# Kernel optimization log

Measured on AMD Instinct MI355X. Metric: run time of the kernel, lower is better.

Reference implementation:

```python
import jax, jax.numpy as jnp
import numpy as np

B, T, N, DM, H, DK, DH = 2, 12, 207, 64, 4, 16, 256


def _build_D_pos(num_heads, length):
    # RetNet-style decay matrix D[h,n,m] = r_h^(n-m) for n>=m, column-sqrt-sum normalized
    r = 1.0 - 2.0 ** (-5.0 - jnp.arange(num_heads, dtype=jnp.float32))
    idx = jnp.arange(length)
    diff = idx[:, None] - idx[None, :]
    mask = diff >= 0
    safe = jnp.where(mask, diff, 0).astype(jnp.float32)
    D = jnp.where(mask, r[:, None, None] ** safe, 0.0)  # [H,T,T]
    D = D / jnp.sqrt(jnp.sum(D, axis=-1, keepdims=True))
    n = jnp.arange(1, length + 1, dtype=jnp.float32)  # theta = 1
    pos = jnp.stack([jnp.cos(n), jnp.sin(n)], axis=0)  # [2,T] = [real, imag]
    return D, pos


def setup_inputs() -> dict:
    key = jax.random.key(0)
    ks = jax.random.split(key, 12)
    xav = lambda k, fi, fo, shp: jax.random.normal(k, shp, jnp.float32) * np.sqrt(2.0 / (fi + fo)).astype(np.float32)
    out2 = 3 * H * DK * DM  # 12288
    return {
        "inputs": jax.random.normal(ks[0], (B, T, N, DM), jnp.float32),
        "c_inputs": jax.random.normal(ks[1], (B, T, N, DM), jnp.float32),
        "ml_w1": xav(ks[2], DM, DH, (DM, DH)),
        "ml_b1": jnp.zeros((DH,), jnp.float32),
        "ml_w2": xav(ks[3], DH, out2, (DH, out2)),
        "ml_b2": jnp.zeros((out2,), jnp.float32),
        "gdc_w1": xav(ks[4], DK, DM, (H, DK, DM)),
        "gdc_w2": xav(ks[5], DK, DM, (H, DK, DM)),
        "wg_w": xav(ks[6], DM, DM, (DM, DM)),
        "wg_b": jnp.zeros((DM,), jnp.float32),
        "wo_w": xav(ks[7], DM, DM, (DM, DM)),
        "wo_b": jnp.zeros((DM,), jnp.float32),
        "ln_g": jnp.ones((DM,), jnp.float32),
        "ln_b": jnp.zeros((DM,), jnp.float32),
        "Num": 0,
    }


def reference(inputs, c_inputs, ml_w1, ml_b1, ml_w2, ml_b2, gdc_w1, gdc_w2,
              wg_w, wg_b, wo_w, wo_b, ln_g, ln_b, Num):
    b, t, n, dm = inputs.shape
    h, dk, _ = gdc_w1.shape
    D, pos = _build_D_pos(h, t)

    # MetaLearner: per-token QKV weight matrices [B,T,N,3,H,dk,dm]
    hid = jax.nn.relu(c_inputs @ ml_w1 + ml_b1)
    W = (hid @ ml_w2 + ml_b2).reshape(b, t, n, 3, h, dk, dm)
    Q = jnp.einsum('btnhkd,btnd->btnhk', W[:, :, :, 0], inputs)
    K = jnp.einsum('btnhkd,btnd->btnhk', W[:, :, :, 1], inputs)
    V = jnp.einsum('btnhkd,btnd->btnhk', W[:, :, :, 2], inputs)

    # complex rotary-like position scaling: leading dim c=2 (real/imag)
    posb = pos[:, :t].reshape(2, 1, t, 1, 1, 1)
    Qp = Q[None] * posb  # [2,B,T,N,H,dk]
    Kp = K[None] * posb

    # retention: sum over c of QK^T / sqrt(dk), decay-masked, abs-sum normalized
    scores = jnp.einsum('cbtnhk,cbsnhk->bnhts', Qp, Kp) / jnp.sqrt(jnp.float32(dk))
    ret = scores * D[None, None]  # [B,N,H,T,T]
    den = jnp.maximum(jnp.abs(jnp.sum(ret, axis=-1, keepdims=True)), 1.0)
    ret = ret / den
    out = jnp.einsum('bnhts,bsnhk->bhtnk', ret, V)  # [B,H,T,N,dk]

    # GroupNorm: normalize over last (dk) axis, nan -> 0
    mu = jnp.mean(out, axis=-1, keepdims=True)
    var = jnp.var(out, axis=-1, keepdims=True)
    out = (out - mu) / jnp.sqrt(var)
    out = jnp.where(jnp.isnan(out), 0.0, out)

    out = 3.0 * jnp.tanh(jnp.swapaxes(out, 0, 1))  # [H,B,T,N,dk]

    # Gated_Dynamic_Connection: softmax over heads per output channel
    x = jnp.transpose(out, (1, 2, 3, 0, 4))  # [B,T,N,H,dk]
    a = jnp.einsum('btnhk,hkm->btnhm', x, gdc_w1)
    s = jax.nn.softmax(jax.nn.relu(jnp.einsum('btnhk,hkm->btnhm', x, gdc_w2)), axis=3)
    g = jnp.einsum('btnhm,btnhm->btnm', a, s)  # [B,T,N,dm]

    # Swish gate + output projection
    z = (inputs @ wg_w + wg_b) * g
    z = z * jax.nn.sigmoid(z)
    o = z @ wo_w + wo_b

    # residual + LayerNorm
    y = o + inputs
    mu2 = jnp.mean(y, axis=-1, keepdims=True)
    var2 = jnp.var(y, axis=-1, keepdims=True)
    y = (y - mu2) / jnp.sqrt(var2 + 1e-5) * ln_g + ln_b
    return y
```

## Files before the change

### kernel.cpp

```cpp
#include <hip/hip_runtime.h>
#include <math.h>

#define B_ 2
#define T_ 12
#define N_ 207
#define DM_ 64
#define H_ 4
#define DK_ 16
#define DH_ 256
#define MTOK 4968
#define MTOKP 4992
#define OUT2 12288
#define QKVC 192
#define RW 512

typedef __bf16 bf16x8 __attribute__((ext_vector_type(8)));
typedef float f32x4 __attribute__((ext_vector_type(4)));
typedef unsigned short ushortx8 __attribute__((ext_vector_type(8)));

__device__ __forceinline__ unsigned short f2bf(float f) {
    union { float f; unsigned u; } v; v.f = f;
    unsigned r = v.u + 0x7fffu + ((v.u >> 16) & 1u);
    return (unsigned short)(r >> 16);
}
__device__ __forceinline__ float bf2f(unsigned short b) {
    union { unsigned u; float f; } v; v.u = ((unsigned)b) << 16; return v.f;
}
__device__ __forceinline__ void gll16(const void* g, void* l) {
    __builtin_amdgcn_global_load_lds((const __attribute__((address_space(1))) void*)g,
                                     (__attribute__((address_space(3))) void*)l, 16, 0, 0);
}

__global__ __launch_bounds__(256) void k_hid2(const float* __restrict__ cin,
                                              const float* __restrict__ w1,
                                              const float* __restrict__ b1,
                                              unsigned short* __restrict__ hid_i) {
    __shared__ float cs[16][DM_];
    const int t0 = blockIdx.x * 16;
    const int tid = threadIdx.x;
    #pragma unroll
    for (int r = 0; r < 4; ++r) {
        int idx = r * 256 + tid;
        int t = idx >> 6, d = idx & 63;
        int tok = t0 + t;
        cs[t][d] = (tok < MTOK) ? cin[(size_t)tok * DM_ + d] : 0.f;
    }
    __syncthreads();
    float a[16];
    #pragma unroll
    for (int t = 0; t < 16; ++t) a[t] = 0.f;
    for (int d = 0; d < DM_; ++d) {
        float wv = w1[d * DH_ + tid];
        #pragma unroll
        for (int t = 0; t < 16; ++t) a[t] = fmaf(cs[t][d], wv, a[t]);
    }
    float b = b1[tid];
    const int g = tid >> 3, pos = tid & 7;
    #pragma unroll
    for (int t = 0; t < 16; ++t) {
        int tok = t0 + t;
        float val = (tok < MTOK) ? fmaxf(a[t] + b, 0.f) : 0.f;
        unsigned short hi = f2bf(val);
        hid_i[(size_t)tok * RW + g * 16 + pos]     = hi;
        hid_i[(size_t)tok * RW + g * 16 + 8 + pos] = f2bf(val - bf2f(hi));
    }
}

__global__ __launch_bounds__(256) void k_split(const float* __restrict__ w2,
                                               unsigned short* __restrict__ wi) {
    __shared__ float tbuf[64][72];
    const int tid = threadIdx.x;
    const int c0 = blockIdx.x * 64;
    const int j0 = blockIdx.y * 64;
    #pragma unroll
    for (int r = 0; r < 4; ++r) {
        int idx = r * 256 + tid;
        int j = idx >> 4, c4 = idx & 15;
        float4 v = *reinterpret_cast<const float4*>(w2 + (size_t)(j0 + j) * OUT2 + c0 + c4 * 4);
        *reinterpret_cast<float4*>(&tbuf[j][c4 * 4]) = v;
    }
    __syncthreads();
    #pragma unroll
    for (int r = 0; r < 2; ++r) {
        int slot = r * 256 + tid;
        int c = slot >> 3, j8 = slot & 7;
        ushortx8 Hv, Lv;
        #pragma unroll
        for (int e = 0; e < 8; ++e) {
            float f = tbuf[j8 * 8 + e][c];
            unsigned short h = f2bf(f);
            Hv[e] = h;
            Lv[e] = f2bf(f - bf2f(h));
        }
        size_t off = (size_t)(c0 + c) * RW + (size_t)(j0 + j8 * 8) * 2;
        *reinterpret_cast<ushortx8*>(wi + off)     = Hv;
        *reinterpret_cast<ushortx8*>(wi + off + 8) = Lv;
    }
}

__global__ __launch_bounds__(256, 4) void k_gemm(const unsigned short* __restrict__ Ai,
                                                 const unsigned short* __restrict__ Bi,
                                                 const float* __restrict__ b2,
                                                 const float* __restrict__ x,
                                                 float* __restrict__ qkv) {
    __shared__ __align__(16) unsigned short sA[8192], sB[8192];
    const int tid = threadIdx.x;
    const int bid = blockIdx.x;
    const int xcd = bid & 7;
    const int r_ = bid >> 3;
    const int m0 = (r_ / 12) * 128;
    const int n0 = (xcd * 12 + (r_ % 12)) * 128;
    const int wid = tid >> 6;
    const int lane = tid & 63;
    const int l15 = lane & 15, l4 = lane >> 4;
    const int wm = wid >> 1, wn = wid & 1;

    const int srow = tid >> 3;
    const int sch  = tid & 7;
    const int gch  = sch ^ (srow & 7);
    const unsigned short* pA = Ai + (size_t)(m0 + srow) * RW + gch * 8;
    const unsigned short* pB = Bi + (size_t)(n0 + srow) * RW + gch * 8;
    const size_t rstep = (size_t)32 * RW;
    const int lbase = wid * 512;

    const int rsw = l15 & 7;
    const int chHi = ((2 * l4) ^ rsw) * 8;
    const int chLo = ((2 * l4 + 1) ^ rsw) * 8;

    f32x4 acc[4][4];
    const f32x4 zero = {0.f, 0.f, 0.f, 0.f};
    #pragma unroll
    for (int i = 0; i < 4; ++i)
        #pragma unroll
        for (int j = 0; j < 4; ++j) acc[i][j] = zero;

    for (int ks = 0; ks < 8; ++ks) {
        #pragma unroll
        for (int i = 0; i < 4; ++i) gll16(pA + i * rstep, &sA[i * 2048 + lbase]);
        #pragma unroll
        for (int i = 0; i < 4; ++i) gll16(pB + i * rstep, &sB[i * 2048 + lbase]);
        pA += 64; pB += 64;
        __syncthreads();

        bf16x8 ah[4], al[4];
        #pragma unroll
        for (int mi = 0; mi < 4; ++mi) {
            int rb = (wm * 64 + mi * 16 + l15) * 64;
            ah[mi] = *reinterpret_cast<const bf16x8*>(&sA[rb + chHi]);
            al[mi] = *reinterpret_cast<const bf16x8*>(&sA[rb + chLo]);
        }
        #pragma unroll
        for (int ni = 0; ni < 4; ++ni) {
            int nb = (wn * 64 + ni * 16 + l15) * 64;
            bf16x8 bh = *reinterpret_cast<const bf16x8*>(&sB[nb + chHi]);
            bf16x8 bl = *reinterpret_cast<const bf16x8*>(&sB[nb + chLo]);
            #pragma unroll
            for (int mi = 0; mi < 4; ++mi)
                acc[mi][ni] = __builtin_amdgcn_mfma_f32_16x16x32_bf16(ah[mi], bh, acc[mi][ni], 0, 0, 0);
            #pragma unroll
            for (int mi = 0; mi < 4; ++mi)
                acc[mi][ni] = __builtin_amdgcn_mfma_f32_16x16x32_bf16(ah[mi], bl, acc[mi][ni], 0, 0, 0);
            #pragma unroll
            for (int mi = 0; mi < 4; ++mi)
                acc[mi][ni] = __builtin_amdgcn_mfma_f32_16x16x32_bf16(al[mi], bh, acc[mi][ni], 0, 0, 0);
        }
        __syncthreads();
    }

    const int cg = (n0 >> 6) + wn;
    float b2v[4];
    #pragma unroll
    for (int ni = 0; ni < 4; ++ni) b2v[ni] = b2[cg * 64 + ni * 16 + l15];
    #pragma unroll
    for (int mi = 0; mi < 4; ++mi) {
        #pragma unroll
        for (int r = 0; r < 4; ++r) {
            int rl = wm * 64 + mi * 16 + l4 * 4 + r;
            int gm = m0 + rl;
            int gmc = gm < MTOK ? gm : MTOK - 1;
            float v = 0.f;
            #pragma unroll
            for (int ni = 0; ni < 4; ++ni)
                v = fmaf(acc[mi][ni][r] + b2v[ni], x[(size_t)gmc * DM_ + ni * 16 + l15], v);
            #pragma unroll
            for (int sw = 1; sw < 16; sw <<= 1) v += __shfl_xor(v, sw, 16);
            if (l15 == 0 && gm < MTOK) qkv[(size_t)gm * QKVC + cg] = v;
        }
    }
}

__global__ __launch_bounds__(256) void k_ret4(const float* __restrict__ qkv,
                                              float* __restrict__ xt) {
    const int tid = threadIdx.x;
    const int g = tid >> 6, lane = tid & 63;
    const int n = blockIdx.x * 4 + g;
    const int h = blockIdx.y;
    const int b = blockIdx.z;
    const bool act = (n < N_);
    __shared__ float Q[4][T_][DK_ + 1], K[4][T_][DK_ + 1], V[4][T_][DK_ + 1];
    __shared__ float ret[4][T_][T_ + 1];
    __shared__ float den[4][T_];
    if (act) {
        for (int idx = lane; idx < T_ * DK_; idx += 64) {
            int t = idx >> 4, k = idx & 15;
            size_t base = ((size_t)((b * T_ + t) * N_ + n)) * QKVC + h * DK_ + k;
            Q[g][t][k] = qkv[base];
            K[g][t][k] = qkv[base + 64];
            V[g][t][k] = qkv[base + 128];
        }
        const float r = 1.f - exp2f(-5.f - (float)h);
        for (int p = lane; p < T_ * T_; p += 64) {
            int t = p / T_, s = p - t * T_;
            float val = 0.f;
            if (s <= t) {
                float dot = 0.f;
                #pragma unroll
                for (int k = 0; k < DK_; ++k) dot = fmaf(Q[g][t][k], K[g][s][k], dot);
                float sum = 0.f, rp = 1.f;
                for (int i = 0; i <= t; ++i) { sum += rp; rp *= r; }
                float Dv = powf(r, (float)(t - s)) / sqrtf(sum);
                val = dot * 0.25f * cosf((float)(t - s)) * Dv;
            }
            ret[g][t][s] = val;
        }
        if (lane < T_) {
            float sm = 0.f;
            for (int j = 0; j < T_; ++j) sm += ret[g][lane][j];
            den[g][lane] = fmaxf(fabsf(sm), 1.f);
        }
        for (int idx = lane; idx < T_ * DK_; idx += 64) {
            int t = idx >> 4, k = idx & 15;
            float o = 0.f;
            for (int s = 0; s <= t; ++s) o = fmaf(ret[g][t][s], V[g][s][k], o);
            o /= den[g][t];
            float mu = o;
            #pragma unroll
            for (int w = 8; w >= 1; w >>= 1) mu += __shfl_xor(mu, w, 16);
            mu *= (1.f / 16.f);
            float dv = o - mu;
            float var = dv * dv;
            #pragma unroll
            for (int w = 8; w >= 1; w >>= 1) var += __shfl_xor(var, w, 16);
            var *= (1.f / 16.f);
            float val = dv / sqrtf(var);
            if (isnan(val)) val = 0.f;
            val = 3.f * tanhf(val);
            xt[((size_t)((b * T_ + t) * N_ + n)) * DM_ + h * DK_ + k] = val;
        }
    }
}

__global__ __launch_bounds__(256) void k_out4(const float* __restrict__ xt,
                                              const float* __restrict__ in,
                                              const float* __restrict__ gw1,
                                              const float* __restrict__ gw2,
                                              const float* __restrict__ wgw,
                                              const float* __restrict__ wgb,
                                              const float* __restrict__ wow,
                                              const float* __restrict__ wob,
                                              const float* __restrict__ lng,
                                              const float* __restrict__ lnb,
                                              float* __restrict__ out) {
    const int tid = threadIdx.x;
    const int w = tid >> 6;
    const int m = tid & 63;
    const int tok = blockIdx.x * 4 + w;
    const bool act = tok < MTOK;
    const int tokc = act ? tok : MTOK - 1;
    __shared__ float xsh[4][DM_], insh[4][DM_], zsh[4][DM_];
    xsh[w][m]  = xt[(size_t)tokc * DM_ + m];
    insh[w][m] = in[(size_t)tokc * DM_ + m];
    float ah[H_], sh[H_];
    #pragma unroll
    for (int h = 0; h < H_; ++h) {
        float a = 0.f, s = 0.f;
        #pragma unroll
        for (int k = 0; k < DK_; ++k) {
            float xv = xsh[w][h * DK_ + k];
            a = fmaf(xv, gw1[(h * DK_ + k) * DM_ + m], a);
            s = fmaf(xv, gw2[(h * DK_ + k) * DM_ + m], s);
        }
        ah[h] = a;
        sh[h] = fmaxf(s, 0.f);
    }
    float mx = fmaxf(fmaxf(sh[0], sh[1]), fmaxf(sh[2], sh[3]));
    float e0 = expf(sh[0] - mx), e1 = expf(sh[1] - mx);
    float e2 = expf(sh[2] - mx), e3 = expf(sh[3] - mx);
    float esum = e0 + e1 + e2 + e3;
    float g = (ah[0] * e0 + ah[1] * e1 + ah[2] * e2 + ah[3] * e3) / esum;
    float z = 0.f;
    for (int d = 0; d < DM_; ++d) z = fmaf(insh[w][d], wgw[d * DM_ + m], z);
    z += wgb[m];
    z *= g;
    z = z / (1.f + expf(-z));
    zsh[w][m] = z;
    float o = 0.f;
    for (int d = 0; d < DM_; ++d) o = fmaf(zsh[w][d], wow[d * DM_ + m], o);
    o += wob[m];
    float y = o + insh[w][m];
    float mu = y;
    #pragma unroll
    for (int xm = 32; xm >= 1; xm >>= 1) mu += __shfl_xor(mu, xm, 64);
    mu *= (1.f / 64.f);
    float dv = y - mu;
    float var = dv * dv;
    #pragma unroll
    for (int xm = 32; xm >= 1; xm >>= 1) var += __shfl_xor(var, xm, 64);
    var *= (1.f / 64.f);
    float res = dv / sqrtf(var + 1e-5f) * lng[m] + lnb[m];
    if (act) out[(size_t)tok * DM_ + m] = res;
}

__global__ __launch_bounds__(256) void k_hid(const float* __restrict__ cin,
                                             const float* __restrict__ w1,
                                             const float* __restrict__ b1,
                                             float* __restrict__ hid) {
    __shared__ float cs[4][DM_];
    const int t0 = blockIdx.x * 4;
    const int tid = threadIdx.x;
    {
        int t = tid >> 6, d = tid & 63;
        cs[t][d] = cin[(size_t)(t0 + t) * DM_ + d];
    }
    __syncthreads();
    float a0 = 0.f, a1 = 0.f, a2 = 0.f, a3 = 0.f;
    for (int d = 0; d < DM_; ++d) {
        float w = w1[d * DH_ + tid];
        a0 = fmaf(cs[0][d], w, a0);
        a1 = fmaf(cs[1][d], w, a1);
        a2 = fmaf(cs[2][d], w, a2);
        a3 = fmaf(cs[3][d], w, a3);
    }
    float b = b1[tid];
    hid[(size_t)(t0 + 0) * DH_ + tid] = fmaxf(a0 + b, 0.f);
    hid[(size_t)(t0 + 1) * DH_ + tid] = fmaxf(a1 + b, 0.f);
    hid[(size_t)(t0 + 2) * DH_ + tid] = fmaxf(a2 + b, 0.f);
    hid[(size_t)(t0 + 3) * DH_ + tid] = fmaxf(a3 + b, 0.f);
}

#define BM 192
#define BN 96
template <int KS>
__global__ __launch_bounds__(256, 2) void k_qkv(const float* __restrict__ x,
                                                const float* __restrict__ hid,
                                                const float* __restrict__ w2,
                                                const float* __restrict__ b2,
                                                float* __restrict__ part) {
    constexpr int JPB = DH_ / KS;
    __shared__ float4 xs4[BM * 16];
    __shared__ float4 ws4[BN * 16];
    const int tid = threadIdx.x;
    const int m0 = blockIdx.x * BM;
    const int c0 = blockIdx.y * BN;
    const int kz = blockIdx.z;
    const int cidx = tid & 15;
    const int midx = tid >> 4;
    #pragma unroll
    for (int i = 0; i < 12; ++i) {
        int e4 = tid + 256 * i;
        int m = e4 >> 4;
        int d4 = e4 & 15;
        int gm = m0 + m;
        float4 v = make_float4(0.f, 0.f, 0.f, 0.f);
        if (gm < MTOK) v = *reinterpret_cast<const float4*>(x + (size_t)gm * DM_ + d4 * 4);
        xs4[m * 16 + (d4 ^ (m & 15))] = v;
    }
    float acc[12][6];
    #pragma unroll
    for (int i = 0; i < 12; ++i)
        #pragma unroll
        for (int q = 0; q < 6; ++q) acc[i][q] = 0.f;
    const int jn = (kz == 0) ? (JPB + 1) : JPB;
    float4 st[6];
    {
        const float* src = w2 + (size_t)(kz * JPB) * OUT2 + c0 * DM_;
        #pragma unroll
        for (int i = 0; i < 6; ++i)
            st[i] = *reinterpret_cast<const float4*>(src + (tid + 256 * i) * 4);
    }
    #pragma unroll
    for (int i = 0; i < 6; ++i) {
        int t4 = tid + 256 * i;
        int c = t4 >> 4;
        int d4 = t4 & 15;
        ws4[c * 16 + (d4 ^ (c & 15))] = st[i];
    }
    __syncthreads();
    for (int jj = 0; jj < jn; ++jj) {
        const bool have_next = (jj + 1 < jn);
        if (have_next) {
            const bool nb = (kz == 0) && (jj + 1 == JPB);
            const float* src = nb ? (b2 + c0 * DM_)
                                  : (w2 + (size_t)(kz * JPB + jj + 1) * OUT2 + c0 * DM_);
            #pragma unroll
            for (int i = 0; i < 6; ++i)
                st[i] = *reinterpret_cast<const float4*>(src + (tid + 256 * i) * 4);
        }
        const bool bias_cur = (kz == 0) && (jj == JPB);
        const int jg = kz * JPB + jj;
        float hv[12];
        #pragma unroll
        for (int i = 0; i < 12; ++i) {
            int gm = m0 + midx + 16 * i;
            hv[i] = bias_cur ? 1.f : ((gm < MTOK) ? hid[(size_t)gm * DH_ + jg] : 0.f);
        }
        for (int d4 = 0; d4 < 16; ++d4) {
            float4 xa[12];
            #pragma unroll
            for (int i = 0; i < 12; ++i) {
                float4 v = xs4[(midx + 16 * i) * 16 + (d4 ^ midx)];
                v.x *= hv[i]; v.y *= hv[i]; v.z *= hv[i]; v.w *= hv[i];
                xa[i] = v;
            }
            #pragma unroll
            for (int q = 0; q < 6; ++q) {
                float4 wv = ws4[(cidx + 16 * q) * 16 + (d4 ^ cidx)];
                #pragma unroll
                for (int i = 0; i < 12; ++i) {
                    float t = acc[i][q];
                    t = fmaf(xa[i].x, wv.x, t);
                    t = fmaf(xa[i].y, wv.y, t);
                    t = fmaf(xa[i].z, wv.z, t);
                    t = fmaf(xa[i].w, wv.w, t);
                    acc[i][q] = t;
                }
            }
        }
        __syncthreads();
        if (have_next) {
            #pragma unroll
            for (int i = 0; i < 6; ++i) {
                int t4 = tid + 256 * i;
                int c = t4 >> 4;
                int d4 = t4 & 15;
                ws4[c * 16 + (d4 ^ (c & 15))] = st[i];
            }
        }
        __syncthreads();
    }
    float* dst = part + (size_t)kz * MTOK * QKVC;
    #pragma unroll
    for (int i = 0; i < 12; ++i) {
        int gm = m0 + midx + 16 * i;
        if (gm < MTOK) {
            #pragma unroll
            for (int q = 0; q < 6; ++q)
                dst[(size_t)gm * QKVC + c0 + cidx + 16 * q] = acc[i][q];
        }
    }
}

template <int KS>
__global__ __launch_bounds__(64) void k_ret(const float* __restrict__ part,
                                            float* __restrict__ xt) {
    const int n = blockIdx.x;
    const int h = blockIdx.y;
    const int b = blockIdx.z;
    const int tid = threadIdx.x;
    __shared__ float Q[T_][DK_ + 1], K[T_][DK_ + 1], V[T_][DK_ + 1];
    __shared__ float ret[T_][T_ + 1];
    __shared__ float den[T_];
    for (int idx = tid; idx < T_ * DK_; idx += 64) {
        int t = idx >> 4, k = idx & 15;
        size_t base = ((size_t)((b * T_ + t) * N_ + n)) * QKVC + h * DK_ + k;
        float q = 0.f, kk = 0.f, v = 0.f;
        #pragma unroll
        for (int p = 0; p < KS; ++p) {
            size_t off = (size_t)p * MTOK * QKVC + base;
            q  += part[off];
            kk += part[off + 64];
            v  += part[off + 128];
        }
        Q[t][k] = q; K[t][k] = kk; V[t][k] = v;
    }
    __syncthreads();
    const float r = 1.f - exp2f(-5.f - (float)h);
    for (int p = tid; p < T_ * T_; p += 64) {
        int t = p / T_, s = p - t * T_;
        float val = 0.f;
        if (s <= t) {
            float dot = 0.f;
            #pragma unroll
            for (int k = 0; k < DK_; ++k) dot = fmaf(Q[t][k], K[s][k], dot);
            float sum = 0.f, rp = 1.f;
            for (int i = 0; i <= t; ++i) { sum += rp; rp *= r; }
            float Dv = powf(r, (float)(t - s)) / sqrtf(sum);
            val = dot * 0.25f * cosf((float)(t - s)) * Dv;
        }
        ret[t][s] = val;
    }
    __syncthreads();
    if (tid < T_) {
        float sm = 0.f;
        for (int j = 0; j < T_; ++j) sm += ret[tid][j];
        den[tid] = fmaxf(fabsf(sm), 1.f);
    }
    __syncthreads();
    for (int idx = tid; idx < T_ * DK_; idx += 64) {
        int t = idx >> 4, k = idx & 15;
        float o = 0.f;
        for (int s = 0; s <= t; ++s) o = fmaf(ret[t][s], V[s][k], o);
        o /= den[t];
        float mu = o;
        #pragma unroll
        for (int w = 8; w >= 1; w >>= 1) mu += __shfl_xor(mu, w, 16);
        mu *= (1.f / 16.f);
        float dv = o - mu;
        float var = dv * dv;
        #pragma unroll
        for (int w = 8; w >= 1; w >>= 1) var += __shfl_xor(var, w, 16);
        var *= (1.f / 16.f);
        float val = dv / sqrtf(var);
        if (isnan(val)) val = 0.f;
        val = 3.f * tanhf(val);
        xt[((size_t)((b * T_ + t) * N_ + n)) * DM_ + h * DK_ + k] = val;
    }
}

extern "C" void kernel_launch(void* const* d_in, const int* in_sizes, int n_in,
                              void* d_out, int out_size, void* d_ws, size_t ws_size,
                              hipStream_t stream) {
    const float* inputs   = (const float*)d_in[0];
    const float* c_inputs = (const float*)d_in[1];
    const float* ml_w1    = (const float*)d_in[2];
    const float* ml_b1    = (const float*)d_in[3];
    const float* ml_w2    = (const float*)d_in[4];
    const float* ml_b2    = (const float*)d_in[5];
    const float* gdc_w1   = (const float*)d_in[6];
    const float* gdc_w2   = (const float*)d_in[7];
    const float* wg_w     = (const float*)d_in[8];
    const float* wg_b     = (const float*)d_in[9];
    const float* wo_w     = (const float*)d_in[10];
    const float* wo_b     = (const float*)d_in[11];
    const float* ln_g     = (const float*)d_in[12];
    const float* ln_b     = (const float*)d_in[13];
    float* out = (float*)d_out;

    const size_t hid_e = (size_t)MTOKP * RW;
    const size_t w2t_e = (size_t)OUT2 * RW;
    const size_t main_bytes = (hid_e + w2t_e) * sizeof(unsigned short)
                            + ((size_t)MTOK * QKVC + (size_t)MTOK * DM_) * sizeof(float);

    if (ws_size >= main_bytes) {
        unsigned short* hid_i = (unsigned short*)d_ws;
        unsigned short* w2t_i = hid_i + hid_e;
        float* qkv = (float*)(w2t_i + w2t_e);
        float* xt  = qkv + (size_t)MTOK * QKVC;

        k_hid2<<<dim3(MTOKP / 16), dim3(256), 0, stream>>>(c_inputs, ml_w1, ml_b1, hid_i);
        k_split<<<dim3(OUT2 / 64, DH_ / 64), dim3(256), 0, stream>>>(ml_w2, w2t_i);
        k_gemm<<<dim3(3744), dim3(256), 0, stream>>>(hid_i, w2t_i, ml_b2, inputs, qkv);
        k_ret4<<<dim3((N_ + 3) / 4, H_, B_), dim3(256), 0, stream>>>(qkv, xt);
        k_out4<<<dim3((MTOK + 3) / 4), dim3(256), 0, stream>>>(xt, inputs, gdc_w1, gdc_w2,
            wg_w, wg_b, wo_w, wo_b, ln_g, ln_b, out);
    } else {
        float* hid  = (float*)d_ws;
        float* xt   = hid + (size_t)MTOK * DH_;
        float* part = xt + (size_t)MTOK * DM_;
        const size_t fixed_f = (size_t)MTOK * DH_ + (size_t)MTOK * DM_;
        auto fits = [&](int ks) {
            return (fixed_f + (size_t)ks * MTOK * QKVC) * sizeof(float) <= ws_size;
        };
        k_hid<<<dim3(MTOK / 4), dim3(256), 0, stream>>>(c_inputs, ml_w1, ml_b1, hid);
        const int gx = (MTOK + BM - 1) / BM;
        if (fits(2)) {
            k_qkv<2><<<dim3(gx, 2, 2), dim3(256), 0, stream>>>(inputs, hid, ml_w2, ml_b2, part);
            k_ret<2><<<dim3(N_, H_, B_), dim3(64), 0, stream>>>(part, xt);
        } else {
            k_qkv<1><<<dim3(gx, 2, 1), dim3(256), 0, stream>>>(inputs, hid, ml_w2, ml_b2, part);
            k_ret<1><<<dim3(N_, H_, B_), dim3(64), 0, stream>>>(part, xt);
        }
        k_out4<<<dim3((MTOK + 3) / 4), dim3(256), 0, stream>>>(xt, inputs, gdc_w1, gdc_w2,
            wg_w, wg_b, wo_w, wo_b, ln_g, ln_b, out);
    }
}
```

Baseline: 131.9 us.

## Fuse retention and output stages into one tail kernel; raise MFMA wave priority

Result: slower. 172.1 us (+30.5%).

```diff
diff --git a/kernel.cpp b/kernel.cpp
--- a/kernel.cpp
+++ b/kernel.cpp
@@ -141,6 +141,7 @@
         for (int i = 0; i < 4; ++i) gll16(pB + i * rstep, &sB[i * 2048 + lbase]);
         pA += 64; pB += 64;
         __syncthreads();
+        __builtin_amdgcn_s_setprio(1);
 
         bf16x8 ah[4], al[4];
         #pragma unroll
@@ -164,6 +165,7 @@
             for (int mi = 0; mi < 4; ++mi)
                 acc[mi][ni] = __builtin_amdgcn_mfma_f32_16x16x32_bf16(al[mi], bh, acc[mi][ni], 0, 0, 0);
         }
+        __builtin_amdgcn_s_setprio(0);
         __syncthreads();
     }
 
@@ -189,64 +191,328 @@
     }
 }
 
-__global__ __launch_bounds__(256) void k_ret4(const float* __restrict__ qkv,
-                                              float* __restrict__ xt) {
-    const int tid = threadIdx.x;
-    const int g = tid >> 6, lane = tid & 63;
-    const int n = blockIdx.x * 4 + g;
+__global__ __launch_bounds__(256) void k_tail(const float* __restrict__ qkv,
+                                              const float* __restrict__ in,
+                                              const float* __restrict__ gw1,
+                                              const float* __restrict__ gw2,
+                                              const float* __restrict__ wgw,
+                                              const float* __restrict__ wgb,
+                                              const float* __restrict__ wow,
+                                              const float* __restrict__ wob,
+                                              const float* __restrict__ lng,
+                                              const float* __restrict__ lnb,
+                                              float* __restrict__ out) {
+    const int n = blockIdx.x;
+    const int b = blockIdx.y;
+    const int tid = threadIdx.x;
+    const int h = tid >> 6;
+    const int lane = tid & 63;
+    __shared__ float Q[H_][T_][DK_ + 1], K[H_][T_][DK_ + 1], V[H_][T_][DK_ + 1];
+    __shared__ float retm[H_][T_][T_ + 1];
+    __shared__ float den[H_][T_];
+    __shared__ float xsh[T_][DM_ + 1], insh[T_][DM_ + 1], zsh[T_][DM_ + 1];
+
+    for (int idx = lane; idx < T_ * DK_; idx += 64) {
+        int t = idx >> 4, k = idx & 15;
+        size_t base = ((size_t)((b * T_ + t) * N_ + n)) * QKVC + h * DK_ + k;
+        Q[h][t][k] = qkv[base];
+        K[h][t][k] = qkv[base + 64];
+        V[h][t][k] = qkv[base + 128];
+    }
+    for (int idx = tid; idx < T_ * DM_; idx += 256) {
+        int t = idx >> 6, d = idx & 63;
+        insh[t][d] = in[((size_t)((b * T_ + t) * N_ + n)) * DM_ + d];
+    }
+
+    const float r = 1.f - exp2f(-5.f - (float)h);
+    for (int p = lane; p < T_ * T_; p += 64) {
+        int t = p / T_, s = p - t * T_;
+        float val = 0.f;
+        if (s <= t) {
+            float dot = 0.f;
+            #pragma unroll
+            for (int k = 0; k < DK_; ++k) dot = fmaf(Q[h][t][k], K[h][s][k], dot);
+            float sum = 0.f, rp = 1.f;
+            for (int i = 0; i <= t; ++i) { sum += rp; rp *= r; }
+            float Dv = powf(r, (float)(t - s)) / sqrtf(sum);
+            val = dot * 0.25f * cosf((float)(t - s)) * Dv;
+        }
+        retm[h][t][s] = val;
+    }
+    if (lane < T_) {
+        float sm = 0.f;
+        for (int j = 0; j < T_; ++j) sm += retm[h][lane][j];
+        den[h][lane] = fmaxf(fabsf(sm), 1.f);
+    }
+    for (int idx = lane; idx < T_ * DK_; idx += 64) {
+        int t = idx >> 4, k = idx & 15;
+        float o = 0.f;
+        for (int s = 0; s <= t; ++s) o = fmaf(retm[h][t][s], V[h][s][k], o);
+        o /= den[h][t];
+        float mu = o;
+        #pragma unroll
+        for (int w = 8; w >= 1; w >>= 1) mu += __shfl_xor(mu, w, 16);
+        mu *= (1.f / 16.f);
+        float dv = o - mu;
+        float var = dv * dv;
+        #pragma unroll
+        for (int w = 8; w >= 1; w >>= 1) var += __shfl_xor(var, w, 16);
+        var *= (1.f / 16.f);
+        float val = dv / sqrtf(var);
+        if (isnan(val)) val = 0.f;
+        xsh[t][h * DK_ + k] = 3.f * tanhf(val);
+    }
+    __syncthreads();
+
+    const int m = lane;
+    #pragma unroll
+    for (int it = 0; it < 3; ++it) {
+        const int t = it * 4 + h;
+        float ah[H_], sh[H_];
+        #pragma unroll
+        for (int hh = 0; hh < H_; ++hh) {
+            float a = 0.f, s = 0.f;
+            #pragma unroll
+            for (int k = 0; k < DK_; ++k) {
+                float xv = xsh[t][hh * DK_ + k];
+                a = fmaf(xv, gw1[(hh * DK_ + k) * DM_ + m], a);
+                s = fmaf(xv, gw2[(hh * DK_ + k) * DM_ + m], s);
+            }
+            ah[hh] = a;
+            sh[hh] = fmaxf(s, 0.f);
+        }
+        float mx = fmaxf(fmaxf(sh[0], sh[1]), fmaxf(sh[2], sh[3]));
+        float e0 = expf(sh[0] - mx), e1 = expf(sh[1] - mx);
+        float e2 = expf(sh[2] - mx), e3 = expf(sh[3] - mx);
+        float esum = e0 + e1 + e2 + e3;
+        float g = (ah[0] * e0 + ah[1] * e1 + ah[2] * e2 + ah[3] * e3) / esum;
+        float z = 0.f;
+        for (int d = 0; d < DM_; ++d) z = fmaf(insh[t][d], wgw[d * DM_ + m], z);
+        z += wgb[m];
+        z *= g;
+        z = z / (1.f + expf(-z));
+        zsh[t][m] = z;
+        float o = 0.f;
+        for (int d = 0; d < DM_; ++d) o = fmaf(zsh[t][d], wow[d * DM_ + m], o);
+        o += wob[m];
+        float y = o + insh[t][m];
+        float mu = y;
+        #pragma unroll
+        for (int xm = 32; xm >= 1; xm >>= 1) mu += __shfl_xor(mu, xm, 64);
+        mu *= (1.f / 64.f);
+        float dv = y - mu;
+        float var = dv * dv;
+        #pragma unroll
+        for (int xm = 32; xm >= 1; xm >>= 1) var += __shfl_xor(var, xm, 64);
+        var *= (1.f / 64.f);
+        out[((size_t)((b * T_ + t) * N_ + n)) * DM_ + m] =
+            dv / sqrtf(var + 1e-5f) * lng[m] + lnb[m];
+    }
+}
+
+__global__ __launch_bounds__(256) void k_hid(const float* __restrict__ cin,
+                                             const float* __restrict__ w1,
+                                             const float* __restrict__ b1,
+                                             float* __restrict__ hid) {
+    __shared__ float cs[4][DM_];
+    const int t0 = blockIdx.x * 4;
+    const int tid = threadIdx.x;
+    {
+        int t = tid >> 6, d = tid & 63;
+        cs[t][d] = cin[(size_t)(t0 + t) * DM_ + d];
+    }
+    __syncthreads();
+    float a0 = 0.f, a1 = 0.f, a2 = 0.f, a3 = 0.f;
+    for (int d = 0; d < DM_; ++d) {
+        float w = w1[d * DH_ + tid];
+        a0 = fmaf(cs[0][d], w, a0);
+        a1 = fmaf(cs[1][d], w, a1);
+        a2 = fmaf(cs[2][d], w, a2);
+        a3 = fmaf(cs[3][d], w, a3);
+    }
+    float b = b1[tid];
+    hid[(size_t)(t0 + 0) * DH_ + tid] = fmaxf(a0 + b, 0.f);
+    hid[(size_t)(t0 + 1) * DH_ + tid] = fmaxf(a1 + b, 0.f);
+    hid[(size_t)(t0 + 2) * DH_ + tid] = fmaxf(a2 + b, 0.f);
+    hid[(size_t)(t0 + 3) * DH_ + tid] = fmaxf(a3 + b, 0.f);
+}
+
+#define BM 192
+#define BN 96
+template <int KS>
+__global__ __launch_bounds__(256, 2) void k_qkv(const float* __restrict__ x,
+                                                const float* __restrict__ hid,
+                                                const float* __restrict__ w2,
+                                                const float* __restrict__ b2,
+                                                float* __restrict__ part) {
+    constexpr int JPB = DH_ / KS;
+    __shared__ float4 xs4[BM * 16];
+    __shared__ float4 ws4[BN * 16];
+    const int tid = threadIdx.x;
+    const int m0 = blockIdx.x * BM;
+    const int c0 = blockIdx.y * BN;
+    const int kz = blockIdx.z;
+    const int cidx = tid & 15;
+    const int midx = tid >> 4;
+    #pragma unroll
+    for (int i = 0; i < 12; ++i) {
+        int e4 = tid + 256 * i;
+        int m = e4 >> 4;
+        int d4 = e4 & 15;
+        int gm = m0 + m;
+        float4 v = make_float4(0.f, 0.f, 0.f, 0.f);
+        if (gm < MTOK) v = *reinterpret_cast<const float4*>(x + (size_t)gm * DM_ + d4 * 4);
+        xs4[m * 16 + (d4 ^ (m & 15))] = v;
+    }
+    float acc[12][6];
+    #pragma unroll
+    for (int i = 0; i < 12; ++i)
+        #pragma unroll
+        for (int q = 0; q < 6; ++q) acc[i][q] = 0.f;
+    const int jn = (kz == 0) ? (JPB + 1) : JPB;
+    float4 st[6];
+    {
+        const float* src = w2 + (size_t)(kz * JPB) * OUT2 + c0 * DM_;
+        #pragma unroll
+        for (int i = 0; i < 6; ++i)
+            st[i] = *reinterpret_cast<const float4*>(src + (tid + 256 * i) * 4);
+    }
+    #pragma unroll
+    for (int i = 0; i < 6; ++i) {
+        int t4 = tid + 256 * i;
+        int c = t4 >> 4;
+        int d4 = t4 & 15;
+        ws4[c * 16 + (d4 ^ (c & 15))] = st[i];
+    }
+    __syncthreads();
+    for (int jj = 0; jj < jn; ++jj) {
+        const bool have_next = (jj + 1 < jn);
+        if (have_next) {
+            const bool nb = (kz == 0) && (jj + 1 == JPB);
+            const float* src = nb ? (b2 + c0 * DM_)
+                                  : (w2 + (size_t)(kz * JPB + jj + 1) * OUT2 + c0 * DM_);
+            #pragma unroll
+            for (int i = 0; i < 6; ++i)
+                st[i] = *reinterpret_cast<const float4*>(src + (tid + 256 * i) * 4);
+        }
+        const bool bias_cur = (kz == 0) && (jj == JPB);
+        const int jg = kz * JPB + jj;
+        float hv[12];
+        #pragma unroll
+        for (int i = 0; i < 12; ++i) {
+            int gm = m0 + midx + 16 * i;
+            hv[i] = bias_cur ? 1.f : ((gm < MTOK) ? hid[(size_t)gm * DH_ + jg] : 0.f);
+        }
+        for (int d4 = 0; d4 < 16; ++d4) {
+            float4 xa[12];
+            #pragma unroll
+            for (int i = 0; i < 12; ++i) {
+                float4 v = xs4[(midx + 16 * i) * 16 + (d4 ^ midx)];
+                v.x *= hv[i]; v.y *= hv[i]; v.z *= hv[i]; v.w *= hv[i];
+                xa[i] = v;
+            }
+            #pragma unroll
+            for (int q = 0; q < 6; ++q) {
+                float4 wv = ws4[(cidx + 16 * q) * 16 + (d4 ^ cidx)];
+                #pragma unroll
+                for (int i = 0; i < 12; ++i) {
+                    float t = acc[i][q];
+                    t = fmaf(xa[i].x, wv.x, t);
+                    t = fmaf(xa[i].y, wv.y, t);
+                    t = fmaf(xa[i].z, wv.z, t);
+                    t = fmaf(xa[i].w, wv.w, t);
+                    acc[i][q] = t;
+                }
+            }
+        }
+        __syncthreads();
+        if (have_next) {
+            #pragma unroll
+            for (int i = 0; i < 6; ++i) {
+                int t4 = tid + 256 * i;
+                int c = t4 >> 4;
+                int d4 = t4 & 15;
+                ws4[c * 16 + (d4 ^ (c & 15))] = st[i];
+            }
+        }
+        __syncthreads();
+    }
+    float* dst = part + (size_t)kz * MTOK * QKVC;
+    #pragma unroll
+    for (int i = 0; i < 12; ++i) {
+        int gm = m0 + midx + 16 * i;
+        if (gm < MTOK) {
+            #pragma unroll
+            for (int q = 0; q < 6; ++q)
+                dst[(size_t)gm * QKVC + c0 + cidx + 16 * q] = acc[i][q];
+        }
+    }
+}
+
+template <int KS>
+__global__ __launch_bounds__(64) void k_ret(const float* __restrict__ part,
+                                            float* __restrict__ xt) {
+    const int n = blockIdx.x;
     const int h = blockIdx.y;
     const int b = blockIdx.z;
-    const bool act = (n < N_);
-    __shared__ float Q[4][T_][DK_ + 1], K[4][T_][DK_ + 1], V[4][T_][DK_ + 1];
-    __shared__ float ret[4][T_][T_ + 1];
-    __shared__ float den[4][T_];
-    if (act) {
-        for (int idx = lane; idx < T_ * DK_; idx += 64) {
-            int t = idx >> 4, k = idx & 15;
-            size_t base = ((size_t)((b * T_ + t) * N_ + n)) * QKVC + h * DK_ + k;
-            Q[g][t][k] = qkv[base];
-            K[g][t][k] = qkv[base + 64];
-            V[g][t][k] = qkv[base + 128];
-        }
-        const float r = 1.f - exp2f(-5.f - (float)h);
-        for (int p = lane; p < T_ * T_; p += 64) {
-            int t = p / T_, s = p - t * T_;
-            float val = 0.f;
-            if (s <= t) {
-                float dot = 0.f;
-                #pragma unroll
-                for (int k = 0; k < DK_; ++k) dot = fmaf(Q[g][t][k], K[g][s][k], dot);
-                float sum = 0.f, rp = 1.f;
-                for (int i = 0; i <= t; ++i) { sum += rp; rp *= r; }
-                float Dv = powf(r, (float)(t - s)) / sqrtf(sum);
-                val = dot * 0.25f * cosf((float)(t - s)) * Dv;
-            }
-            ret[g][t][s] = val;
-        }
-        if (lane < T_) {
-            float sm = 0.f;
-            for (int j = 0; j < T_; ++j) sm += ret[g][lane][j];
-            den[g][lane] = fmaxf(fabsf(sm), 1.f);
-        }
-        for (int idx = lane; idx < T_ * DK_; idx += 64) {
-            int t = idx >> 4, k = idx & 15;
-            float o = 0.f;
-            for (int s = 0; s <= t; ++s) o = fmaf(ret[g][t][s], V[g][s][k], o);
-            o /= den[g][t];
-            float mu = o;
-            #pragma unroll
-            for (int w = 8; w >= 1; w >>= 1) mu += __shfl_xor(mu, w, 16);
-            mu *= (1.f / 16.f);
-            float dv = o - mu;
-            float var = dv * dv;
-            #pragma unroll
-            for (int w = 8; w >= 1; w >>= 1) var += __shfl_xor(var, w, 16);
-            var *= (1.f / 16.f);
-            float val = dv / sqrtf(var);
-            if (isnan(val)) val = 0.f;
-            val = 3.f * tanhf(val);
-            xt[((size_t)((b * T_ + t) * N_ + n)) * DM_ + h * DK_ + k] = val;
-        }
+    const int tid = threadIdx.x;
+    __shared__ float Q[T_][DK_ + 1], K[T_][DK_ + 1], V[T_][DK_ + 1];
+    __shared__ float ret[T_][T_ + 1];
+    __shared__ float den[T_];
+    for (int idx = tid; idx < T_ * DK_; idx += 64) {
+        int t = idx >> 4, k = idx & 15;
+        size_t base = ((size_t)((b * T_ + t) * N_ + n)) * QKVC + h * DK_ + k;
+        float q = 0.f, kk = 0.f, v = 0.f;
+        #pragma unroll
+        for (int p = 0; p < KS; ++p) {
+            size_t off = (size_t)p * MTOK * QKVC + base;
+            q  += part[off];
+            kk += part[off + 64];
+            v  += part[off + 128];
+        }
+        Q[t][k] = q; K[t][k] = kk; V[t][k] = v;
+    }
+    __syncthreads();
+    const float r = 1.f - exp2f(-5.f - (float)h);
+    for (int p = tid; p < T_ * T_; p += 64) {
+        int t = p / T_, s = p - t * T_;
+        float val = 0.f;
+        if (s <= t) {
+            float dot = 0.f;
+            #pragma unroll
+            for (int k = 0; k < DK_; ++k) dot = fmaf(Q[t][k], K[s][k], dot);
+            float sum = 0.f, rp = 1.f;
+            for (int i = 0; i <= t; ++i) { sum += rp; rp *= r; }
+            float Dv = powf(r, (float)(t - s)) / sqrtf(sum);
+            val = dot * 0.25f * cosf((float)(t - s)) * Dv;
+        }
+        ret[t][s] = val;
+    }
+    __syncthreads();
+    if (tid < T_) {
+        float sm = 0.f;
+        for (int j = 0; j < T_; ++j) sm += ret[tid][j];
+        den[tid] = fmaxf(fabsf(sm), 1.f);
+    }
+    __syncthreads();
+    for (int idx = tid; idx < T_ * DK_; idx += 64) {
+        int t = idx >> 4, k = idx & 15;
+        float o = 0.f;
+        for (int s = 0; s <= t; ++s) o = fmaf(ret[t][s], V[s][k], o);
+        o /= den[t];
+        float mu = o;
+        #pragma unroll
+        for (int w = 8; w >= 1; w >>= 1) mu += __shfl_xor(mu, w, 16);
+        mu *= (1.f / 16.f);
+        float dv = o - mu;
+        float var = dv * dv;
+        #pragma unroll
+        for (int w = 8; w >= 1; w >>= 1) var += __shfl_xor(var, w, 16);
+        var *= (1.f / 16.f);
+        float val = dv / sqrtf(var);
+        if (isnan(val)) val = 0.f;
+        val = 3.f * tanhf(val);
+        xt[((size_t)((b * T_ + t) * N_ + n)) * DM_ + h * DK_ + k] = val;
     }
 }
 
@@ -309,212 +575,6 @@
     var *= (1.f / 64.f);
     float res = dv / sqrtf(var + 1e-5f) * lng[m] + lnb[m];
     if (act) out[(size_t)tok * DM_ + m] = res;
-}
-
-__global__ __launch_bounds__(256) void k_hid(const float* __restrict__ cin,
-                                             const float* __restrict__ w1,
-                                             const float* __restrict__ b1,
-                                             float* __restrict__ hid) {
-    __shared__ float cs[4][DM_];
-    const int t0 = blockIdx.x * 4;
-    const int tid = threadIdx.x;
-    {
-        int t = tid >> 6, d = tid & 63;
-        cs[t][d] = cin[(size_t)(t0 + t) * DM_ + d];
-    }
-    __syncthreads();
-    float a0 = 0.f, a1 = 0.f, a2 = 0.f, a3 = 0.f;
-    for (int d = 0; d < DM_; ++d) {
-        float w = w1[d * DH_ + tid];
-        a0 = fmaf(cs[0][d], w, a0);
-        a1 = fmaf(cs[1][d], w, a1);
-        a2 = fmaf(cs[2][d], w, a2);
-        a3 = fmaf(cs[3][d], w, a3);
-    }
-    float b = b1[tid];
-    hid[(size_t)(t0 + 0) * DH_ + tid] = fmaxf(a0 + b, 0.f);
-    hid[(size_t)(t0 + 1) * DH_ + tid] = fmaxf(a1 + b, 0.f);
-    hid[(size_t)(t0 + 2) * DH_ + tid] = fmaxf(a2 + b, 0.f);
-    hid[(size_t)(t0 + 3) * DH_ + tid] = fmaxf(a3 + b, 0.f);
-}
-
-#define BM 192
-#define BN 96
-template <int KS>
-__global__ __launch_bounds__(256, 2) void k_qkv(const float* __restrict__ x,
-                                                const float* __restrict__ hid,
-                                                const float* __restrict__ w2,
-                                                const float* __restrict__ b2,
-                                                float* __restrict__ part) {
-    constexpr int JPB = DH_ / KS;
-    __shared__ float4 xs4[BM * 16];
-    __shared__ float4 ws4[BN * 16];
-    const int tid = threadIdx.x;
-    const int m0 = blockIdx.x * BM;
-    const int c0 = blockIdx.y * BN;
-    const int kz = blockIdx.z;
-    const int cidx = tid & 15;
-    const int midx = tid >> 4;
-    #pragma unroll
-    for (int i = 0; i < 12; ++i) {
-        int e4 = tid + 256 * i;
-        int m = e4 >> 4;
-        int d4 = e4 & 15;
-        int gm = m0 + m;
-        float4 v = make_float4(0.f, 0.f, 0.f, 0.f);
-        if (gm < MTOK) v = *reinterpret_cast<const float4*>(x + (size_t)gm * DM_ + d4 * 4);
-        xs4[m * 16 + (d4 ^ (m & 15))] = v;
-    }
-    float acc[12][6];
-    #pragma unroll
-    for (int i = 0; i < 12; ++i)
-        #pragma unroll
-        for (int q = 0; q < 6; ++q) acc[i][q] = 0.f;
-    const int jn = (kz == 0) ? (JPB + 1) : JPB;
-    float4 st[6];
-    {
-        const float* src = w2 + (size_t)(kz * JPB) * OUT2 + c0 * DM_;
-        #pragma unroll
-        for (int i = 0; i < 6; ++i)
-            st[i] = *reinterpret_cast<const float4*>(src + (tid + 256 * i) * 4);
-    }
-    #pragma unroll
-    for (int i = 0; i < 6; ++i) {
-        int t4 = tid + 256 * i;
-        int c = t4 >> 4;
-        int d4 = t4 & 15;
-        ws4[c * 16 + (d4 ^ (c & 15))] = st[i];
-    }
-    __syncthreads();
-    for (int jj = 0; jj < jn; ++jj) {
-        const bool have_next = (jj + 1 < jn);
-        if (have_next) {
-            const bool nb = (kz == 0) && (jj + 1 == JPB);
-            const float* src = nb ? (b2 + c0 * DM_)
-                                  : (w2 + (size_t)(kz * JPB + jj + 1) * OUT2 + c0 * DM_);
-            #pragma unroll
-            for (int i = 0; i < 6; ++i)
-                st[i] = *reinterpret_cast<const float4*>(src + (tid + 256 * i) * 4);
-        }
-        const bool bias_cur = (kz == 0) && (jj == JPB);
-        const int jg = kz * JPB + jj;
-        float hv[12];
-        #pragma unroll
-        for (int i = 0; i < 12; ++i) {
-            int gm = m0 + midx + 16 * i;
-            hv[i] = bias_cur ? 1.f : ((gm < MTOK) ? hid[(size_t)gm * DH_ + jg] : 0.f);
-        }
-        for (int d4 = 0; d4 < 16; ++d4) {
-            float4 xa[12];
-            #pragma unroll
-            for (int i = 0; i < 12; ++i) {
-                float4 v = xs4[(midx + 16 * i) * 16 + (d4 ^ midx)];
-                v.x *= hv[i]; v.y *= hv[i]; v.z *= hv[i]; v.w *= hv[i];
-                xa[i] = v;
-            }
-            #pragma unroll
-            for (int q = 0; q < 6; ++q) {
-                float4 wv = ws4[(cidx + 16 * q) * 16 + (d4 ^ cidx)];
-                #pragma unroll
-                for (int i = 0; i < 12; ++i) {
-                    float t = acc[i][q];
-                    t = fmaf(xa[i].x, wv.x, t);
-                    t = fmaf(xa[i].y, wv.y, t);
-                    t = fmaf(xa[i].z, wv.z, t);
-                    t = fmaf(xa[i].w, wv.w, t);
-                    acc[i][q] = t;
-                }
-            }
-        }
-        __syncthreads();
-        if (have_next) {
-            #pragma unroll
-            for (int i = 0; i < 6; ++i) {
-                int t4 = tid + 256 * i;
-                int c = t4 >> 4;
-                int d4 = t4 & 15;
-                ws4[c * 16 + (d4 ^ (c & 15))] = st[i];
-            }
-        }
-        __syncthreads();
-    }
-    float* dst = part + (size_t)kz * MTOK * QKVC;
-    #pragma unroll
-    for (int i = 0; i < 12; ++i) {
-        int gm = m0 + midx + 16 * i;
-        if (gm < MTOK) {
-            #pragma unroll
-            for (int q = 0; q < 6; ++q)
-                dst[(size_t)gm * QKVC + c0 + cidx + 16 * q] = acc[i][q];
-        }
-    }
-}
-
-template <int KS>
-__global__ __launch_bounds__(64) void k_ret(const float* __restrict__ part,
-                                            float* __restrict__ xt) {
-    const int n = blockIdx.x;
-    const int h = blockIdx.y;
-    const int b = blockIdx.z;
-    const int tid = threadIdx.x;
-    __shared__ float Q[T_][DK_ + 1], K[T_][DK_ + 1], V[T_][DK_ + 1];
-    __shared__ float ret[T_][T_ + 1];
-    __shared__ float den[T_];
-    for (int idx = tid; idx < T_ * DK_; idx += 64) {
-        int t = idx >> 4, k = idx & 15;
-        size_t base = ((size_t)((b * T_ + t) * N_ + n)) * QKVC + h * DK_ + k;
-        float q = 0.f, kk = 0.f, v = 0.f;
-        #pragma unroll
-        for (int p = 0; p < KS; ++p) {
-            size_t off = (size_t)p * MTOK * QKVC + base;
-            q  += part[off];
-            kk += part[off + 64];
-            v  += part[off + 128];
-        }
-        Q[t][k] = q; K[t][k] = kk; V[t][k] = v;
-    }
-    __syncthreads();
-    const float r = 1.f - exp2f(-5.f - (float)h);
-    for (int p = tid; p < T_ * T_; p += 64) {
-        int t = p / T_, s = p - t * T_;
-        float val = 0.f;
-        if (s <= t) {
-            float dot = 0.f;
-            #pragma unroll
-            for (int k = 0; k < DK_; ++k) dot = fmaf(Q[t][k], K[s][k], dot);
-            float sum = 0.f, rp = 1.f;
-            for (int i = 0; i <= t; ++i) { sum += rp; rp *= r; }
-            float Dv = powf(r, (float)(t - s)) / sqrtf(sum);
-            val = dot * 0.25f * cosf((float)(t - s)) * Dv;
-        }
-        ret[t][s] = val;
-    }
-    __syncthreads();
-    if (tid < T_) {
-        float sm = 0.f;
-        for (int j = 0; j < T_; ++j) sm += ret[tid][j];
-        den[tid] = fmaxf(fabsf(sm), 1.f);
-    }
-    __syncthreads();
-    for (int idx = tid; idx < T_ * DK_; idx += 64) {
-        int t = idx >> 4, k = idx & 15;
-        float o = 0.f;
-        for (int s = 0; s <= t; ++s) o = fmaf(ret[t][s], V[s][k], o);
-        o /= den[t];
-        float mu = o;
-        #pragma unroll
-        for (int w = 8; w >= 1; w >>= 1) mu += __shfl_xor(mu, w, 16);
-        mu *= (1.f / 16.f);
-        float dv = o - mu;
-        float var = dv * dv;
-        #pragma unroll
-        for (int w = 8; w >= 1; w >>= 1) var += __shfl_xor(var, w, 16);
-        var *= (1.f / 16.f);
-        float val = dv / sqrtf(var);
-        if (isnan(val)) val = 0.f;
-        val = 3.f * tanhf(val);
-        xt[((size_t)((b * T_ + t) * N_ + n)) * DM_ + h * DK_ + k] = val;
-    }
 }
 
 extern "C" void kernel_launch(void* const* d_in, const int* in_sizes, int n_in,
@@ -539,19 +599,17 @@
     const size_t hid_e = (size_t)MTOKP * RW;
     const size_t w2t_e = (size_t)OUT2 * RW;
     const size_t main_bytes = (hid_e + w2t_e) * sizeof(unsigned short)
-                            + ((size_t)MTOK * QKVC + (size_t)MTOK * DM_) * sizeof(float);
+                            + ((size_t)MTOK * QKVC) * sizeof(float);
 
     if (ws_size >= main_bytes) {
         unsigned short* hid_i = (unsigned short*)d_ws;
         unsigned short* w2t_i = hid_i + hid_e;
         float* qkv = (float*)(w2t_i + w2t_e);
-        float* xt  = qkv + (size_t)MTOK * QKVC;
 
         k_hid2<<<dim3(MTOKP / 16), dim3(256), 0, stream>>>(c_inputs, ml_w1, ml_b1, hid_i);
         k_split<<<dim3(OUT2 / 64, DH_ / 64), dim3(256), 0, stream>>>(ml_w2, w2t_i);
         k_gemm<<<dim3(3744), dim3(256), 0, stream>>>(hid_i, w2t_i, ml_b2, inputs, qkv);
-        k_ret4<<<dim3((N_ + 3) / 4, H_, B_), dim3(256), 0, stream>>>(qkv, xt);
-        k_out4<<<dim3((MTOK + 3) / 4), dim3(256), 0, stream>>>(xt, inputs, gdc_w1, gdc_w2,
+        k_tail<<<dim3(N_, B_), dim3(256), 0, stream>>>(qkv, inputs, gdc_w1, gdc_w2,
             wg_w, wg_b, wo_w, wo_b, ln_g, ln_b, out);
     } else {
         float* hid  = (float*)d_ws;
```
